# Kernel tuning notes

Hardware: AMD Instinct MI355X
Metric: run time of the kernel (lower is better)

The kernel has to match this reference:

```python
import jax, jax.numpy as jnp
import numpy as np

N = 100000   # nodes
E = 1600000  # edges (avg degree 16)
D = 128      # in_channels == hidden_channels
H = 4        # heads
C = D // H   # per-head channels = 32


def leaky(x, slope):
    return jnp.where(x >= 0, x, slope * x)


def setup_inputs() -> dict:
    key = jax.random.key(0)
    ks = jax.random.split(key, 12)
    s = 1.0 / np.sqrt(D)
    return {
        "x": jax.random.normal(ks[0], (N, D), jnp.float32),
        "edge_index": jax.random.randint(ks[1], (2, E), 0, N, jnp.int32),
        "edge_type": jax.random.randint(ks[2], (E,), 0, 8, jnp.int32),
        # linear1 (first_layer=True): LeakyReLU(0.01) -> Linear(D, D)
        "W1": jax.random.normal(ks[3], (D, D), jnp.float32) * s,
        "b1": jnp.zeros((D,), jnp.float32),
        # GATConv params: lin (no bias), att_src/att_dst [1,H,C], output bias [H*C]
        "Wg": jax.random.normal(ks[4], (D, D), jnp.float32) * s,
        "att_src": jax.random.normal(ks[5], (1, H, C), jnp.float32) * s,
        "att_dst": jax.random.normal(ks[6], (1, H, C), jnp.float32) * s,
        "bias_g": jnp.zeros((D,), jnp.float32),
        # linear2: LeakyReLU(0.01) -> Linear(D, D)
        "W2": jax.random.normal(ks[7], (D, D), jnp.float32) * s,
        "b2": jnp.zeros((D,), jnp.float32),
    }


def reference(x, edge_index, edge_type, W1, b1, Wg, att_src, att_dst, bias_g, W2, b2):
    # dropout layers act in eval mode (identity); edge_type is unused by forward.
    # linear1: LeakyReLU(0.01) then Linear
    x = leaky(x, 0.01) @ W1.T + b1                      # [N, D]

    # GATConv (add_self_loops=False, concat heads)
    h = (x @ Wg.T).reshape(N, H, C)                     # [N, H, C]
    a_src = jnp.sum(h * att_src, axis=-1)               # [N, H]
    a_dst = jnp.sum(h * att_dst, axis=-1)               # [N, H]

    src, dst = edge_index[0], edge_index[1]
    alpha = leaky(a_src[src] + a_dst[dst], 0.2)          # [E, H]

    # segment softmax over destination nodes (numerically stable)
    amax = jax.ops.segment_max(alpha, dst, num_segments=N)   # [N, H], -inf for empty
    amax = jnp.where(jnp.isfinite(amax), amax, 0.0)
    ex = jnp.exp(alpha - amax[dst])                      # [E, H]
    denom = jax.ops.segment_sum(ex, dst, num_segments=N) # [N, H]
    coeff = ex / (denom[dst] + 1e-16)                    # [E, H]

    msg = h[src] * coeff[:, :, None]                     # [E, H, C]
    out = jax.ops.segment_sum(msg, dst, num_segments=N)  # [N, H, C]
    out = out.reshape(N, H * C) + bias_g                 # [N, D]

    # linear2: LeakyReLU(0.01) then Linear; Dropout(0.3) identity at eval
    out = leaky(out, 0.01) @ W2.T + b2                   # [N, D]
    return out
```

## Files before the change

kernel.cpp:

```cpp
#include <hip/hip_runtime.h>
#include <hip/hip_bf16.h>

#define D128 128

typedef __attribute__((ext_vector_type(8))) short bf16x8;
typedef __attribute__((ext_vector_type(4))) float f32x4;

__device__ __forceinline__ float b2f(unsigned short u) {
    union { unsigned int i; float f; } z;
    z.i = ((unsigned int)u) << 16;
    return z.f;
}

__device__ __forceinline__ unsigned short f2b(float f) {
    union { float f; unsigned int i; } z;
    z.f = f;
    unsigned int r = z.i + 0x7FFFu + ((z.i >> 16) & 1u);
    return (unsigned short)(r >> 16);
}

__device__ __forceinline__ f32x4 mfma16(bf16x8 a, bf16x8 b, f32x4 c) {
    return __builtin_amdgcn_mfma_f32_16x16x32_bf16(a, b, c, 0, 0, 0);
}

#define CHUNK 8192
#define MAXBINS 512
#define BINCAP 8192
#define XBB 1536

__global__ __launch_bounds__(256) void k_prep1(
    const float* __restrict__ x,
    const float* __restrict__ W1, const float* __restrict__ Wg,
    const float* __restrict__ b1,
    const int* __restrict__ ei, int* __restrict__ M,
    float* __restrict__ Wc, float* __restrict__ bc,
    unsigned short* __restrict__ xb,
    int N, int E, int B, int nbins)
{
    __shared__ float wgr[256];
    __shared__ int hist[MAXBINS];
    const int t = threadIdx.x;
    if (blockIdx.x < 64) {
        const int i0 = blockIdx.x * 2;
        wgr[t] = Wg[i0 * 128 + t];
        __syncthreads();
        const int half = t >> 7;
        const int j = t & 127;
        const float* wr = &wgr[half * 128];
        float acc = 0.f;
        #pragma unroll 4
        for (int k = 0; k < 128; ++k)
            acc += wr[k] * W1[k * 128 + j];
        Wc[(i0 + half) * 128 + j] = acc;
        if (j == 0) {
            float ab = 0.f;
            for (int k = 0; k < 128; ++k) ab += wr[k] * b1[k];
            bc[i0 + half] = ab;
        }
    } else if (blockIdx.x < 64 + B) {
        const int chunk = blockIdx.x - 64;
        for (int i = t; i < nbins; i += 256) hist[i] = 0;
        __syncthreads();
        const int base = chunk * CHUNK;
        const int end = min(base + CHUNK, E);
        for (int e = base + t; e < end; e += 256)
            atomicAdd(&hist[ei[E + e] >> 8], 1);
        __syncthreads();
        for (int i = t; i < nbins; i += 256)
            M[i * B + chunk] = hist[i];
    } else {
        const size_t total = (size_t)N * 128;
        const size_t stride = (size_t)XBB * 256 * 8;
        for (size_t i = ((size_t)(blockIdx.x - 64 - B) * 256 + t) * 8; i + 8 <= total; i += stride) {
            float4 f0 = *(const float4*)(x + i);
            float4 f1 = *(const float4*)(x + i + 4);
            float v[8] = { f0.x, f0.y, f0.z, f0.w, f1.x, f1.y, f1.z, f1.w };
            union { uint4 q; unsigned short s[8]; } o;
            #pragma unroll
            for (int jj = 0; jj < 8; ++jj) {
                float f = v[jj];
                f = f >= 0.f ? f : 0.01f * f;
                o.s[jj] = f2b(f);
            }
            *(uint4*)(xb + i) = o.q;
        }
    }
}

__global__ __launch_bounds__(256) void k_prep2(
    const float* __restrict__ Wc, const float* __restrict__ bc,
    const float* __restrict__ att_s, const float* __restrict__ att_d,
    const float* __restrict__ W2,
    unsigned short* __restrict__ Wcat, unsigned short* __restrict__ W2l,
    float* __restrict__ lbias)
{
    const int b = blockIdx.x, t = threadIdx.x;
    if (b < 9) {
        const int q = b * 256 + t;
        const int ct = q >> 8, rem = q & 255;
        const int ks = rem >> 6, lane = rem & 63;
        const int ldiv = lane >> 4, lmod = lane & 15;
        const int kb = ks * 32 + ldiv * 8;
        float v[8];
        if (ct < 8) {
            const int rho = ct * 16 + lmod;
            const float4 a = *(const float4*)(Wc + rho * 128 + kb);
            const float4 bq = *(const float4*)(Wc + rho * 128 + kb + 4);
            v[0] = a.x; v[1] = a.y; v[2] = a.z; v[3] = a.w;
            v[4] = bq.x; v[5] = bq.y; v[6] = bq.z; v[7] = bq.w;
        } else {
            #pragma unroll
            for (int e = 0; e < 8; ++e) v[e] = 0.f;
            if (lmod < 8) {
                const int hh = lmod & 3;
                const float* av = lmod < 4 ? att_s : att_d;
                for (int c = 0; c < 32; ++c) {
                    const float w = av[hh * 32 + c];
                    const float* wrow = Wc + (hh * 32 + c) * 128 + kb;
                    #pragma unroll
                    for (int e = 0; e < 8; ++e) v[e] += w * wrow[e];
                }
            }
        }
        union { uint4 qq; unsigned short s[8]; } o;
        #pragma unroll
        for (int e = 0; e < 8; ++e) o.s[e] = f2b(v[e]);
        *(uint4*)(Wcat + q * 8) = o.qq;
    } else if (b < 17) {
        const int q = (b - 9) * 256 + t;
        const int ct = q >> 8, rem = q & 255;
        const int ks = rem >> 6, lane = rem & 63;
        const int ldiv = lane >> 4, lmod = lane & 15;
        const int kb = ks * 32 + ldiv * 8;
        const int rho = ct * 16 + lmod;
        const float4 a = *(const float4*)(W2 + rho * 128 + kb);
        const float4 bq = *(const float4*)(W2 + rho * 128 + kb + 4);
        union { uint4 qq; unsigned short s[8]; } o;
        o.s[0] = f2b(a.x); o.s[1] = f2b(a.y); o.s[2] = f2b(a.z); o.s[3] = f2b(a.w);
        o.s[4] = f2b(bq.x); o.s[5] = f2b(bq.y); o.s[6] = f2b(bq.z); o.s[7] = f2b(bq.w);
        *(uint4*)(W2l + q * 8) = o.qq;
    } else {
        if (t < 144) {
            float v = 0.f;
            if (t < 128) v = bc[t];
            else if (t < 136) {
                const int hh = (t - 128) & 3;
                const float* av = t < 132 ? att_s : att_d;
                for (int c = 0; c < 32; ++c) v += av[hh * 32 + c] * bc[hh * 32 + c];
            }
            lbias[t] = v;
        }
    }
}

__global__ __launch_bounds__(256) void k_gemm_h(
    const unsigned short* __restrict__ xb,
    const unsigned short* __restrict__ Wcat,
    const float* __restrict__ lbias,
    unsigned short* __restrict__ hfeat,
    float* __restrict__ asrc, float* __restrict__ adst, int N)
{
    __shared__ __align__(16) unsigned short sW[18432];
    const int t = threadIdx.x;
    const int wave = t >> 6, lane = t & 63, lmod = lane & 15, ldiv = lane >> 4;
    const int rowBase = blockIdx.x * 64;

    uint4 w[9];
    #pragma unroll
    for (int r = 0; r < 9; ++r)
        w[r] = *(const uint4*)(Wcat + r * 2048 + t * 8);

    int row = rowBase + wave * 16 + lmod;
    row = min(row, N - 1);
    bf16x8 afr[4];
    #pragma unroll
    for (int ks = 0; ks < 4; ++ks)
        afr[ks] = *(const bf16x8*)(xb + (size_t)row * D128 + ks * 32 + ldiv * 8);

    #pragma unroll
    for (int r = 0; r < 9; ++r)
        *(uint4*)&sW[r * 2048 + t * 8] = w[r];
    __syncthreads();

    f32x4 acc[9] = {};
    #pragma unroll
    for (int ct = 0; ct < 9; ++ct) {
        #pragma unroll
        for (int ks = 0; ks < 4; ++ks) {
            bf16x8 bfr = *(const bf16x8*)&sW[(ct * 256 + ks * 64 + lane) * 8];
            acc[ct] = mfma16(afr[ks], bfr, acc[ct]);
        }
    }

    const int orow = rowBase + wave * 16 + ldiv * 4;
    #pragma unroll
    for (int ct = 0; ct < 8; ++ct) {
        const int col = ct * 16 + lmod;
        const float bias = lbias[col];
        #pragma unroll
        for (int r = 0; r < 4; ++r)
            if (orow + r < N)
                hfeat[(size_t)(orow + r) * D128 + col] = f2b(acc[ct][r] + bias);
    }
    if (lmod < 8) {
        const float lb = lbias[128 + lmod];
        float* dst = lmod < 4 ? asrc : adst;
        const int hh = lmod & 3;
        #pragma unroll
        for (int r = 0; r < 4; ++r)
            if (orow + r < N)
                dst[(size_t)(orow + r) * 4 + hh] = acc[8][r] + lb;
    }
}

__global__ __launch_bounds__(1024) void k_scan1(
    const int* __restrict__ in, int* __restrict__ scanned,
    int* __restrict__ bsum, int n)
{
    __shared__ int lds[1024];
    const int gid = blockIdx.x * 1024 + threadIdx.x;
    const int v = gid < n ? in[gid] : 0;
    lds[threadIdx.x] = v;
    __syncthreads();
    #pragma unroll
    for (int off = 1; off < 1024; off <<= 1) {
        int t = threadIdx.x >= off ? lds[threadIdx.x - off] : 0;
        __syncthreads();
        lds[threadIdx.x] += t;
        __syncthreads();
    }
    if (gid < n) scanned[gid] = lds[threadIdx.x] - v;
    if (threadIdx.x == 1023) bsum[blockIdx.x] = lds[1023];
}

__global__ __launch_bounds__(256) void kA2(
    const int* __restrict__ ei, const int* __restrict__ scanned,
    const int* __restrict__ bsum, int2* __restrict__ binned,
    int E, int B, int nbins, int nM)
{
    __shared__ int cursor[MAXBINS];
    __shared__ int bpre[1024];
    const int nsb = (nM + 1023) >> 10;
    for (int i = threadIdx.x; i < nsb; i += 256) bpre[i] = bsum[i];
    __syncthreads();
    if (threadIdx.x == 0) {
        int run = 0;
        for (int i = 0; i < nsb; ++i) { int tv = bpre[i]; bpre[i] = run; run += tv; }
    }
    __syncthreads();
    for (int i = threadIdx.x; i < nbins; i += 256) {
        const int idx = i * B + blockIdx.x;
        cursor[i] = scanned[idx] + bpre[idx >> 10];
    }
    __syncthreads();
    const int base = blockIdx.x * CHUNK;
    const int end = min(base + CHUNK, E);
    for (int e = base + threadIdx.x; e < end; e += 256) {
        const int s = ei[e], d = ei[E + e];
        const int pos = atomicAdd(&cursor[d >> 8], 1);
        binned[pos] = make_int2(s, d);
    }
}

__global__ __launch_bounds__(256) void kB(
    const int2* __restrict__ binned, const int* __restrict__ scanned,
    const int* __restrict__ bsum, int* __restrict__ bucket,
    int* __restrict__ rowstart, int* __restrict__ rowend,
    int E, int B, int nbins, int N, int nM)
{
    __shared__ int2 eb[BINCAP];
    __shared__ int ldeg[256];
    __shared__ int lscan[256];
    __shared__ int lcur[256];
    __shared__ int bpre[1024];
    const int nsb = (nM + 1023) >> 10;
    for (int i = threadIdx.x; i < nsb; i += 256) bpre[i] = bsum[i];
    __syncthreads();
    if (threadIdx.x == 0) {
        int run = 0;
        for (int i = 0; i < nsb; ++i) { int tv = bpre[i]; bpre[i] = run; run += tv; }
    }
    __syncthreads();
    const int bin = blockIdx.x;
    const int i0 = bin * B;
    const int binstart = scanned[i0] + bpre[i0 >> 10];
    int binend;
    if (bin + 1 < nbins) {
        const int i1 = (bin + 1) * B;
        binend = scanned[i1] + bpre[i1 >> 10];
    } else {
        binend = E;
    }
    int n = binend - binstart;
    if (n > BINCAP) n = BINCAP;

    for (int i = threadIdx.x; i < n; i += 256) eb[i] = binned[binstart + i];
    ldeg[threadIdx.x] = 0;
    __syncthreads();
    for (int i = threadIdx.x; i < n; i += 256)
        atomicAdd(&ldeg[eb[i].y & 255], 1);
    __syncthreads();
    const int v = ldeg[threadIdx.x];
    lscan[threadIdx.x] = v;
    __syncthreads();
    #pragma unroll
    for (int off = 1; off < 256; off <<= 1) {
        int t = threadIdx.x >= off ? lscan[threadIdx.x - off] : 0;
        __syncthreads();
        lscan[threadIdx.x] += t;
        __syncthreads();
    }
    const int excl = lscan[threadIdx.x] - v;
    lcur[threadIdx.x] = excl;
    const int d = (bin << 8) + threadIdx.x;
    if (d < N) {
        rowstart[d] = binstart + excl;
        rowend[d]   = binstart + excl + v;
    }
    __syncthreads();
    for (int i = threadIdx.x; i < n; i += 256) {
        const int lp = atomicAdd(&lcur[eb[i].y & 255], 1);
        bucket[binstart + lp] = eb[i].x;
    }
}

__global__ __launch_bounds__(256) void k_gat(
    const int* __restrict__ bucket,
    const int* __restrict__ rowstart, const int* __restrict__ rowend,
    const float* __restrict__ asrc, const float* __restrict__ adst,
    const unsigned short* __restrict__ hfeat,
    const float* __restrict__ bias_g,
    unsigned short* __restrict__ outbf, int N)
{
    const int wave = threadIdx.x >> 6;
    const int lane = threadIdx.x & 63;
    const int g    = lane >> 4;
    const int gl   = lane & 15;
    const int h    = gl >> 2;
    const int d    = blockIdx.x * 16 + wave * 4 + g;

    int start = 0, end = 0;
    float a_d = 0.f;
    if (d < N) {
        start = rowstart[d];
        end   = rowend[d];
        a_d   = adst[(size_t)d * 4 + h];
    }
    const unsigned int chb = (unsigned int)(gl << 3);
    const unsigned short* hbase = hfeat + chb;

    float acc[8] = {0.f, 0.f, 0.f, 0.f, 0.f, 0.f, 0.f, 0.f};
    float denom = 0.f;

    int j = start;
    for (; j + 4 <= end; j += 4) {
        const int s0 = bucket[j];
        const int s1 = bucket[j + 1];
        const int s2 = bucket[j + 2];
        const int s3 = bucket[j + 3];
        const float as0 = asrc[((size_t)s0 << 2) + h];
        const float as1 = asrc[((size_t)s1 << 2) + h];
        const float as2 = asrc[((size_t)s2 << 2) + h];
        const float as3 = asrc[((size_t)s3 << 2) + h];
        const uint4 hp0 = *(const uint4*)(hbase + ((unsigned int)s0 << 7));
        const uint4 hp1 = *(const uint4*)(hbase + ((unsigned int)s1 << 7));
        const uint4 hp2 = *(const uint4*)(hbase + ((unsigned int)s2 << 7));
        const uint4 hp3 = *(const uint4*)(hbase + ((unsigned int)s3 << 7));
        float a0 = as0 + a_d; a0 = a0 >= 0.f ? a0 : 0.2f * a0;
        float a1 = as1 + a_d; a1 = a1 >= 0.f ? a1 : 0.2f * a1;
        float a2 = as2 + a_d; a2 = a2 >= 0.f ? a2 : 0.2f * a2;
        float a3 = as3 + a_d; a3 = a3 >= 0.f ? a3 : 0.2f * a3;
        const float w0 = __expf(a0), w1 = __expf(a1);
        const float w2 = __expf(a2), w3 = __expf(a3);
        denom += (w0 + w1) + (w2 + w3);
        acc[0] += w0 * b2f((unsigned short)(hp0.x & 0xFFFFu)) + w1 * b2f((unsigned short)(hp1.x & 0xFFFFu))
                + w2 * b2f((unsigned short)(hp2.x & 0xFFFFu)) + w3 * b2f((unsigned short)(hp3.x & 0xFFFFu));
        acc[1] += w0 * b2f((unsigned short)(hp0.x >> 16))     + w1 * b2f((unsigned short)(hp1.x >> 16))
                + w2 * b2f((unsigned short)(hp2.x >> 16))     + w3 * b2f((unsigned short)(hp3.x >> 16));
        acc[2] += w0 * b2f((unsigned short)(hp0.y & 0xFFFFu)) + w1 * b2f((unsigned short)(hp1.y & 0xFFFFu))
                + w2 * b2f((unsigned short)(hp2.y & 0xFFFFu)) + w3 * b2f((unsigned short)(hp3.y & 0xFFFFu));
        acc[3] += w0 * b2f((unsigned short)(hp0.y >> 16))     + w1 * b2f((unsigned short)(hp1.y >> 16))
                + w2 * b2f((unsigned short)(hp2.y >> 16))     + w3 * b2f((unsigned short)(hp3.y >> 16));
        acc[4] += w0 * b2f((unsigned short)(hp0.z & 0xFFFFu)) + w1 * b2f((unsigned short)(hp1.z & 0xFFFFu))
                + w2 * b2f((unsigned short)(hp2.z & 0xFFFFu)) + w3 * b2f((unsigned short)(hp3.z & 0xFFFFu));
        acc[5] += w0 * b2f((unsigned short)(hp0.z >> 16))     + w1 * b2f((unsigned short)(hp1.z >> 16))
                + w2 * b2f((unsigned short)(hp2.z >> 16))     + w3 * b2f((unsigned short)(hp3.z >> 16));
        acc[6] += w0 * b2f((unsigned short)(hp0.w & 0xFFFFu)) + w1 * b2f((unsigned short)(hp1.w & 0xFFFFu))
                + w2 * b2f((unsigned short)(hp2.w & 0xFFFFu)) + w3 * b2f((unsigned short)(hp3.w & 0xFFFFu));
        acc[7] += w0 * b2f((unsigned short)(hp0.w >> 16))     + w1 * b2f((unsigned short)(hp1.w >> 16))
                + w2 * b2f((unsigned short)(hp2.w >> 16))     + w3 * b2f((unsigned short)(hp3.w >> 16));
    }
    for (; j < end; ++j) {
        const int s0 = bucket[j];
        const float as0 = asrc[((size_t)s0 << 2) + h];
        const uint4 hp0 = *(const uint4*)(hbase + ((unsigned int)s0 << 7));
        float a0 = as0 + a_d; a0 = a0 >= 0.f ? a0 : 0.2f * a0;
        const float w0 = __expf(a0);
        denom += w0;
        acc[0] += w0 * b2f((unsigned short)(hp0.x & 0xFFFFu));
        acc[1] += w0 * b2f((unsigned short)(hp0.x >> 16));
        acc[2] += w0 * b2f((unsigned short)(hp0.y & 0xFFFFu));
        acc[3] += w0 * b2f((unsigned short)(hp0.y >> 16));
        acc[4] += w0 * b2f((unsigned short)(hp0.z & 0xFFFFu));
        acc[5] += w0 * b2f((unsigned short)(hp0.z >> 16));
        acc[6] += w0 * b2f((unsigned short)(hp0.w & 0xFFFFu));
        acc[7] += w0 * b2f((unsigned short)(hp0.w >> 16));
    }

    if (d < N) {
        const float inv = 1.f / (denom + 1e-16f);
        const float4 bg0 = *(const float4*)(bias_g + chb);
        const float4 bg1 = *(const float4*)(bias_g + chb + 4);
        const float bg[8] = { bg0.x, bg0.y, bg0.z, bg0.w, bg1.x, bg1.y, bg1.z, bg1.w };
        unsigned short s[8];
        #pragma unroll
        for (int k2 = 0; k2 < 8; ++k2) {
            float v = acc[k2] * inv + bg[k2];
            v = v >= 0.f ? v : 0.01f * v;
            s[k2] = f2b(v);
        }
        uint4 o;
        o.x = ((unsigned int)s[1] << 16) | s[0];
        o.y = ((unsigned int)s[3] << 16) | s[2];
        o.z = ((unsigned int)s[5] << 16) | s[4];
        o.w = ((unsigned int)s[7] << 16) | s[6];
        *(uint4*)(outbf + (((unsigned int)d << 7) + chb)) = o;
    }
}

__global__ __launch_bounds__(256) void k_final(
    const unsigned short* __restrict__ gatbf,
    const unsigned short* __restrict__ W2l,
    const float* __restrict__ b2,
    float* __restrict__ out, int N)
{
    __shared__ __align__(16) unsigned short sW[16384];
    const int t = threadIdx.x;
    const int wave = t >> 6, lane = t & 63, lmod = lane & 15, ldiv = lane >> 4;
    const int rowBase = blockIdx.x * 64;

    uint4 w[8];
    #pragma unroll
    for (int r = 0; r < 8; ++r)
        w[r] = *(const uint4*)(W2l + r * 2048 + t * 8);

    int row = rowBase + wave * 16 + lmod;
    row = min(row, N - 1);
    bf16x8 afr[4];
    #pragma unroll
    for (int ks = 0; ks < 4; ++ks)
        afr[ks] = *(const bf16x8*)(gatbf + (size_t)row * D128 + ks * 32 + ldiv * 8);

    #pragma unroll
    for (int r = 0; r < 8; ++r)
        *(uint4*)&sW[r * 2048 + t * 8] = w[r];
    __syncthreads();

    f32x4 acc[8] = {};
    #pragma unroll
    for (int ct = 0; ct < 8; ++ct) {
        #pragma unroll
        for (int ks = 0; ks < 4; ++ks) {
            bf16x8 bfr = *(const bf16x8*)&sW[(ct * 256 + ks * 64 + lane) * 8];
            acc[ct] = mfma16(afr[ks], bfr, acc[ct]);
        }
    }

    const int orow = rowBase + wave * 16 + ldiv * 4;
    #pragma unroll
    for (int ct = 0; ct < 8; ++ct) {
        const int col = ct * 16 + lmod;
        const float bb = b2[col];
        #pragma unroll
        for (int r = 0; r < 4; ++r)
            if (orow + r < N)
                out[(size_t)(orow + r) * D128 + col] = acc[ct][r] + bb;
    }
}

extern "C" void kernel_launch(void* const* d_in, const int* in_sizes, int n_in,
                              void* d_out, int out_size, void* d_ws, size_t ws_size,
                              hipStream_t stream)
{
    const float* x    = (const float*)d_in[0];
    const int*   ei   = (const int*)d_in[1];
    const float* W1   = (const float*)d_in[3];
    const float* b1   = (const float*)d_in[4];
    const float* Wg   = (const float*)d_in[5];
    const float* atts = (const float*)d_in[6];
    const float* attd = (const float*)d_in[7];
    const float* bg   = (const float*)d_in[8];
    const float* W2   = (const float*)d_in[9];
    const float* b2   = (const float*)d_in[10];
    float* out = (float*)d_out;

    const int N = in_sizes[0] / D128;
    const int E = in_sizes[1] / 2;

    const int B     = (E + CHUNK - 1) / CHUNK;
    const int nbins = (N + 255) >> 8;
    const int nM    = nbins * B;

    char* ws = (char*)d_ws;
    float* Wc = (float*)ws;
    size_t off = 65536;
    float* bc    = (float*)(ws + off); off += 512;
    float* lbias = (float*)(ws + off); off += 1024;
    unsigned short* Wcat = (unsigned short*)(ws + off); off += 36864;
    unsigned short* W2l  = (unsigned short*)(ws + off); off += 32768;
    unsigned short* xb   = (unsigned short*)(ws + off); off += (size_t)N * D128 * 2;
    unsigned short* hfeat = (unsigned short*)(ws + off); off += (size_t)N * D128 * 2;
    float* asrc = (float*)(ws + off); off += (size_t)N * 4 * 4;
    float* adst = (float*)(ws + off); off += (size_t)N * 4 * 4;
    int* M       = (int*)(ws + off); off += (size_t)nM * 4;
    int* scanned = (int*)(ws + off); off += (size_t)nM * 4;
    int* bsum    = (int*)(ws + off); off += 1024 * 4;
    int2* binned = (int2*)(ws + off); off += (size_t)E * 8;
    int* bucket  = (int*)(ws + off); off += (size_t)E * 4;
    int* rowstart = (int*)(ws + off); off += (size_t)N * 4;
    int* rowend   = (int*)(ws + off); off += (size_t)N * 4;
    unsigned short* outbf = (unsigned short*)(ws + off); off += (size_t)N * D128 * 2;

    k_prep1<<<64 + B + XBB, 256, 0, stream>>>(x, W1, Wg, b1, ei, M, Wc, bc, xb,
                                              N, E, B, nbins);
    k_prep2<<<18, 256, 0, stream>>>(Wc, bc, atts, attd, W2, Wcat, W2l, lbias);

    const int nbg = (N + 63) / 64;
    k_gemm_h<<<nbg, 256, 0, stream>>>(xb, Wcat, lbias, hfeat, asrc, adst, N);

    const int nsb = (nM + 1023) / 1024;
    k_scan1<<<nsb, 1024, 0, stream>>>(M, scanned, bsum, nM);
    kA2<<<B, 256, 0, stream>>>(ei, scanned, bsum, binned, E, B, nbins, nM);
    kB<<<nbins, 256, 0, stream>>>(binned, scanned, bsum, bucket,
                                  rowstart, rowend, E, B, nbins, N, nM);

    k_gat<<<(N + 15) / 16, 256, 0, stream>>>(bucket, rowstart, rowend,
                                             asrc, adst, hfeat, bg, outbf, N);

    k_final<<<nbg, 256, 0, stream>>>(outbf, W2l, b2, out, N);
}
```

Baseline: 302.6 us.

## Merge scan into prep2, merge GEMM with edge binning, unroll-by-2 GAT loop

The scan kernel is folded into the weight-prep kernel as extra 256-thread blocks that each scan 1024 entries, four per thread. The h-projection GEMM and the edge-binning pass are fused into one launch that dispatches on block index. This removes two kernel launches and lets independent work overlap. The GAT aggregation loop goes from 4-way to 2-way unrolling with nontemporal bucket loads, trading memory-level parallelism for fewer registers, and the fused kernel's 36KB LDS footprint also applies to the binning blocks.

```diff
diff --git a/kernel.cpp b/kernel.cpp
--- a/kernel.cpp
+++ b/kernel.cpp
@@ -87,13 +87,16 @@
     }
 }
 
-__global__ __launch_bounds__(256) void k_prep2(
+__global__ __launch_bounds__(256) void k_prep2s(
     const float* __restrict__ Wc, const float* __restrict__ bc,
     const float* __restrict__ att_s, const float* __restrict__ att_d,
     const float* __restrict__ W2,
     unsigned short* __restrict__ Wcat, unsigned short* __restrict__ W2l,
-    float* __restrict__ lbias)
-{
+    float* __restrict__ lbias,
+    const int* __restrict__ M, int* __restrict__ scanned,
+    int* __restrict__ bsum, int nM)
+{
+    __shared__ int lds[256];
     const int b = blockIdx.x, t = threadIdx.x;
     if (b < 9) {
         const int q = b * 256 + t;
@@ -139,7 +142,7 @@
         o.s[0] = f2b(a.x); o.s[1] = f2b(a.y); o.s[2] = f2b(a.z); o.s[3] = f2b(a.w);
         o.s[4] = f2b(bq.x); o.s[5] = f2b(bq.y); o.s[6] = f2b(bq.z); o.s[7] = f2b(bq.w);
         *(uint4*)(W2l + q * 8) = o.qq;
-    } else {
+    } else if (b == 17) {
         if (t < 144) {
             float v = 0.f;
             if (t < 128) v = bc[t];
@@ -150,115 +153,122 @@
             }
             lbias[t] = v;
         }
-    }
-}
-
-__global__ __launch_bounds__(256) void k_gemm_h(
+    } else {
+        const int sid = b - 18;
+        const int g0 = sid * 1024 + t * 4;
+        int v0 = g0     < nM ? M[g0]     : 0;
+        int v1 = g0 + 1 < nM ? M[g0 + 1] : 0;
+        int v2 = g0 + 2 < nM ? M[g0 + 2] : 0;
+        int v3 = g0 + 3 < nM ? M[g0 + 3] : 0;
+        const int s = v0 + v1 + v2 + v3;
+        lds[t] = s;
+        __syncthreads();
+        #pragma unroll
+        for (int off = 1; off < 256; off <<= 1) {
+            int tv = t >= off ? lds[t - off] : 0;
+            __syncthreads();
+            lds[t] += tv;
+            __syncthreads();
+        }
+        int run = lds[t] - s;
+        if (g0     < nM) scanned[g0]     = run;
+        run += v0;
+        if (g0 + 1 < nM) scanned[g0 + 1] = run;
+        run += v1;
+        if (g0 + 2 < nM) scanned[g0 + 2] = run;
+        run += v2;
+        if (g0 + 3 < nM) scanned[g0 + 3] = run;
+        if (t == 255) bsum[sid] = lds[255];
+    }
+}
+
+__global__ __launch_bounds__(256) void k_gemmA2(
     const unsigned short* __restrict__ xb,
     const unsigned short* __restrict__ Wcat,
     const float* __restrict__ lbias,
     unsigned short* __restrict__ hfeat,
-    float* __restrict__ asrc, float* __restrict__ adst, int N)
-{
-    __shared__ __align__(16) unsigned short sW[18432];
-    const int t = threadIdx.x;
-    const int wave = t >> 6, lane = t & 63, lmod = lane & 15, ldiv = lane >> 4;
-    const int rowBase = blockIdx.x * 64;
-
-    uint4 w[9];
-    #pragma unroll
-    for (int r = 0; r < 9; ++r)
-        w[r] = *(const uint4*)(Wcat + r * 2048 + t * 8);
-
-    int row = rowBase + wave * 16 + lmod;
-    row = min(row, N - 1);
-    bf16x8 afr[4];
-    #pragma unroll
-    for (int ks = 0; ks < 4; ++ks)
-        afr[ks] = *(const bf16x8*)(xb + (size_t)row * D128 + ks * 32 + ldiv * 8);
-
-    #pragma unroll
-    for (int r = 0; r < 9; ++r)
-        *(uint4*)&sW[r * 2048 + t * 8] = w[r];
-    __syncthreads();
-
-    f32x4 acc[9] = {};
-    #pragma unroll
-    for (int ct = 0; ct < 9; ++ct) {
-        #pragma unroll
-        for (int ks = 0; ks < 4; ++ks) {
-            bf16x8 bfr = *(const bf16x8*)&sW[(ct * 256 + ks * 64 + lane) * 8];
-            acc[ct] = mfma16(afr[ks], bfr, acc[ct]);
-        }
-    }
-
-    const int orow = rowBase + wave * 16 + ldiv * 4;
-    #pragma unroll
-    for (int ct = 0; ct < 8; ++ct) {
-        const int col = ct * 16 + lmod;
-        const float bias = lbias[col];
-        #pragma unroll
-        for (int r = 0; r < 4; ++r)
-            if (orow + r < N)
-                hfeat[(size_t)(orow + r) * D128 + col] = f2b(acc[ct][r] + bias);
-    }
-    if (lmod < 8) {
-        const float lb = lbias[128 + lmod];
-        float* dst = lmod < 4 ? asrc : adst;
-        const int hh = lmod & 3;
-        #pragma unroll
-        for (int r = 0; r < 4; ++r)
-            if (orow + r < N)
-                dst[(size_t)(orow + r) * 4 + hh] = acc[8][r] + lb;
-    }
-}
-
-__global__ __launch_bounds__(1024) void k_scan1(
-    const int* __restrict__ in, int* __restrict__ scanned,
-    int* __restrict__ bsum, int n)
-{
-    __shared__ int lds[1024];
-    const int gid = blockIdx.x * 1024 + threadIdx.x;
-    const int v = gid < n ? in[gid] : 0;
-    lds[threadIdx.x] = v;
-    __syncthreads();
-    #pragma unroll
-    for (int off = 1; off < 1024; off <<= 1) {
-        int t = threadIdx.x >= off ? lds[threadIdx.x - off] : 0;
-        __syncthreads();
-        lds[threadIdx.x] += t;
-        __syncthreads();
-    }
-    if (gid < n) scanned[gid] = lds[threadIdx.x] - v;
-    if (threadIdx.x == 1023) bsum[blockIdx.x] = lds[1023];
-}
-
-__global__ __launch_bounds__(256) void kA2(
+    float* __restrict__ asrc, float* __restrict__ adst,
     const int* __restrict__ ei, const int* __restrict__ scanned,
     const int* __restrict__ bsum, int2* __restrict__ binned,
-    int E, int B, int nbins, int nM)
-{
-    __shared__ int cursor[MAXBINS];
-    __shared__ int bpre[1024];
-    const int nsb = (nM + 1023) >> 10;
-    for (int i = threadIdx.x; i < nsb; i += 256) bpre[i] = bsum[i];
-    __syncthreads();
-    if (threadIdx.x == 0) {
-        int run = 0;
-        for (int i = 0; i < nsb; ++i) { int tv = bpre[i]; bpre[i] = run; run += tv; }
-    }
-    __syncthreads();
-    for (int i = threadIdx.x; i < nbins; i += 256) {
-        const int idx = i * B + blockIdx.x;
-        cursor[i] = scanned[idx] + bpre[idx >> 10];
-    }
-    __syncthreads();
-    const int base = blockIdx.x * CHUNK;
-    const int end = min(base + CHUNK, E);
-    for (int e = base + threadIdx.x; e < end; e += 256) {
-        const int s = ei[e], d = ei[E + e];
-        const int pos = atomicAdd(&cursor[d >> 8], 1);
-        binned[pos] = make_int2(s, d);
+    int N, int E, int B, int nbins, int nM, int nbg)
+{
+    __shared__ __align__(16) unsigned char smem[36864];
+    const int t = threadIdx.x;
+    if (blockIdx.x < nbg) {
+        unsigned short* sW = (unsigned short*)smem;
+        const int wave = t >> 6, lane = t & 63, lmod = lane & 15, ldiv = lane >> 4;
+        const int rowBase = blockIdx.x * 64;
+
+        uint4 w[9];
+        #pragma unroll
+        for (int r = 0; r < 9; ++r)
+            w[r] = *(const uint4*)(Wcat + r * 2048 + t * 8);
+
+        int row = rowBase + wave * 16 + lmod;
+        row = min(row, N - 1);
+        bf16x8 afr[4];
+        #pragma unroll
+        for (int ks = 0; ks < 4; ++ks)
+            afr[ks] = *(const bf16x8*)(xb + (size_t)row * D128 + ks * 32 + ldiv * 8);
+
+        #pragma unroll
+        for (int r = 0; r < 9; ++r)
+            *(uint4*)&sW[r * 2048 + t * 8] = w[r];
+        __syncthreads();
+
+        f32x4 acc[9] = {};
+        #pragma unroll
+        for (int ct = 0; ct < 9; ++ct) {
+            #pragma unroll
+            for (int ks = 0; ks < 4; ++ks) {
+                bf16x8 bfr = *(const bf16x8*)&sW[(ct * 256 + ks * 64 + lane) * 8];
+                acc[ct] = mfma16(afr[ks], bfr, acc[ct]);
+            }
+        }
+
+        const int orow = rowBase + wave * 16 + ldiv * 4;
+        #pragma unroll
+        for (int ct = 0; ct < 8; ++ct) {
+            const int col = ct * 16 + lmod;
+            const float bias = lbias[col];
+            #pragma unroll
+            for (int r = 0; r < 4; ++r)
+                if (orow + r < N)
+                    hfeat[(size_t)(orow + r) * D128 + col] = f2b(acc[ct][r] + bias);
+        }
+        if (lmod < 8) {
+            const float lb = lbias[128 + lmod];
+            float* dst = lmod < 4 ? asrc : adst;
+            const int hh = lmod & 3;
+            #pragma unroll
+            for (int r = 0; r < 4; ++r)
+                if (orow + r < N)
+                    dst[(size_t)(orow + r) * 4 + hh] = acc[8][r] + lb;
+        }
+    } else {
+        int* cursor = (int*)smem;
+        int* bpre   = (int*)(smem + MAXBINS * 4);
+        const int chunk = blockIdx.x - nbg;
+        const int nsb = (nM + 1023) >> 10;
+        for (int i = t; i < nsb; i += 256) bpre[i] = bsum[i];
+        __syncthreads();
+        if (t == 0) {
+            int run = 0;
+            for (int i = 0; i < nsb; ++i) { int tv = bpre[i]; bpre[i] = run; run += tv; }
+        }
+        __syncthreads();
+        for (int i = t; i < nbins; i += 256) {
+            const int idx = i * B + chunk;
+            cursor[i] = scanned[idx] + bpre[idx >> 10];
+        }
+        __syncthreads();
+        const int base = chunk * CHUNK;
+        const int end = min(base + CHUNK, E);
+        for (int e = base + t; e < end; e += 256) {
+            const int s = ei[e], d = ei[E + e];
+            const int pos = atomicAdd(&cursor[d >> 8], 1);
+            binned[pos] = make_int2(s, d);
+        }
     }
 }
 
@@ -305,9 +315,9 @@
     __syncthreads();
     #pragma unroll
     for (int off = 1; off < 256; off <<= 1) {
-        int t = threadIdx.x >= off ? lscan[threadIdx.x - off] : 0;
-        __syncthreads();
-        lscan[threadIdx.x] += t;
+        int tv = threadIdx.x >= off ? lscan[threadIdx.x - off] : 0;
+        __syncthreads();
+        lscan[threadIdx.x] += tv;
         __syncthreads();
     }
     const int excl = lscan[threadIdx.x] - v;
@@ -353,45 +363,28 @@
     float denom = 0.f;
 
     int j = start;
-    for (; j + 4 <= end; j += 4) {
-        const int s0 = bucket[j];
-        const int s1 = bucket[j + 1];
-        const int s2 = bucket[j + 2];
-        const int s3 = bucket[j + 3];
+    for (; j + 2 <= end; j += 2) {
+        const int s0 = __builtin_nontemporal_load(bucket + j);
+        const int s1 = __builtin_nontemporal_load(bucket + j + 1);
         const float as0 = asrc[((size_t)s0 << 2) + h];
         const float as1 = asrc[((size_t)s1 << 2) + h];
-        const float as2 = asrc[((size_t)s2 << 2) + h];
-        const float as3 = asrc[((size_t)s3 << 2) + h];
         const uint4 hp0 = *(const uint4*)(hbase + ((unsigned int)s0 << 7));
         const uint4 hp1 = *(const uint4*)(hbase + ((unsigned int)s1 << 7));
-        const uint4 hp2 = *(const uint4*)(hbase + ((unsigned int)s2 << 7));
-        const uint4 hp3 = *(const uint4*)(hbase + ((unsigned int)s3 << 7));
         float a0 = as0 + a_d; a0 = a0 >= 0.f ? a0 : 0.2f * a0;
         float a1 = as1 + a_d; a1 = a1 >= 0.f ? a1 : 0.2f * a1;
-        float a2 = as2 + a_d; a2 = a2 >= 0.f ? a2 : 0.2f * a2;
-        float a3 = as3 + a_d; a3 = a3 >= 0.f ? a3 : 0.2f * a3;
         const float w0 = __expf(a0), w1 = __expf(a1);
-        const float w2 = __expf(a2), w3 = __expf(a3);
-        denom += (w0 + w1) + (w2 + w3);
-        acc[0] += w0 * b2f((unsigned short)(hp0.x & 0xFFFFu)) + w1 * b2f((unsigned short)(hp1.x & 0xFFFFu))
-                + w2 * b2f((unsigned short)(hp2.x & 0xFFFFu)) + w3 * b2f((unsigned short)(hp3.x & 0xFFFFu));
-        acc[1] += w0 * b2f((unsigned short)(hp0.x >> 16))     + w1 * b2f((unsigned short)(hp1.x >> 16))
-                + w2 * b2f((unsigned short)(hp2.x >> 16))     + w3 * b2f((unsigned short)(hp3.x >> 16));
-        acc[2] += w0 * b2f((unsigned short)(hp0.y & 0xFFFFu)) + w1 * b2f((unsigned short)(hp1.y & 0xFFFFu))
-                + w2 * b2f((unsigned short)(hp2.y & 0xFFFFu)) + w3 * b2f((unsigned short)(hp3.y & 0xFFFFu));
-        acc[3] += w0 * b2f((unsigned short)(hp0.y >> 16))     + w1 * b2f((unsigned short)(hp1.y >> 16))
-                + w2 * b2f((unsigned short)(hp2.y >> 16))     + w3 * b2f((unsigned short)(hp3.y >> 16));
-        acc[4] += w0 * b2f((unsigned short)(hp0.z & 0xFFFFu)) + w1 * b2f((unsigned short)(hp1.z & 0xFFFFu))
-                + w2 * b2f((unsigned short)(hp2.z & 0xFFFFu)) + w3 * b2f((unsigned short)(hp3.z & 0xFFFFu));
-        acc[5] += w0 * b2f((unsigned short)(hp0.z >> 16))     + w1 * b2f((unsigned short)(hp1.z >> 16))
-                + w2 * b2f((unsigned short)(hp2.z >> 16))     + w3 * b2f((unsigned short)(hp3.z >> 16));
-        acc[6] += w0 * b2f((unsigned short)(hp0.w & 0xFFFFu)) + w1 * b2f((unsigned short)(hp1.w & 0xFFFFu))
-                + w2 * b2f((unsigned short)(hp2.w & 0xFFFFu)) + w3 * b2f((unsigned short)(hp3.w & 0xFFFFu));
-        acc[7] += w0 * b2f((unsigned short)(hp0.w >> 16))     + w1 * b2f((unsigned short)(hp1.w >> 16))
-                + w2 * b2f((unsigned short)(hp2.w >> 16))     + w3 * b2f((unsigned short)(hp3.w >> 16));
-    }
-    for (; j < end; ++j) {
-        const int s0 = bucket[j];
+        denom += w0 + w1;
+        acc[0] += w0 * b2f((unsigned short)(hp0.x & 0xFFFFu)) + w1 * b2f((unsigned short)(hp1.x & 0xFFFFu));
+        acc[1] += w0 * b2f((unsigned short)(hp0.x >> 16))     + w1 * b2f((unsigned short)(hp1.x >> 16));
+        acc[2] += w0 * b2f((unsigned short)(hp0.y & 0xFFFFu)) + w1 * b2f((unsigned short)(hp1.y & 0xFFFFu));
+        acc[3] += w0 * b2f((unsigned short)(hp0.y >> 16))     + w1 * b2f((unsigned short)(hp1.y >> 16));
+        acc[4] += w0 * b2f((unsigned short)(hp0.z & 0xFFFFu)) + w1 * b2f((unsigned short)(hp1.z & 0xFFFFu));
+        acc[5] += w0 * b2f((unsigned short)(hp0.z >> 16))     + w1 * b2f((unsigned short)(hp1.z >> 16));
+        acc[6] += w0 * b2f((unsigned short)(hp0.w & 0xFFFFu)) + w1 * b2f((unsigned short)(hp1.w & 0xFFFFu));
+        acc[7] += w0 * b2f((unsigned short)(hp0.w >> 16))     + w1 * b2f((unsigned short)(hp1.w >> 16));
+    }
+    if (j < end) {
+        const int s0 = __builtin_nontemporal_load(bucket + j);
         const float as0 = asrc[((size_t)s0 << 2) + h];
         const uint4 hp0 = *(const uint4*)(hbase + ((unsigned int)s0 << 7));
         float a0 = as0 + a_d; a0 = a0 >= 0.f ? a0 : 0.2f * a0;
@@ -500,6 +493,7 @@
     const int B     = (E + CHUNK - 1) / CHUNK;
     const int nbins = (N + 255) >> 8;
     const int nM    = nbins * B;
+    const int nsb   = (nM + 1023) / 1024;
 
     char* ws = (char*)d_ws;
     float* Wc = (float*)ws;
@@ -523,19 +517,15 @@
 
     k_prep1<<<64 + B + XBB, 256, 0, stream>>>(x, W1, Wg, b1, ei, M, Wc, bc, xb,
                                               N, E, B, nbins);
-    k_prep2<<<18, 256, 0, stream>>>(Wc, bc, atts, attd, W2, Wcat, W2l, lbias);
-
+    k_prep2s<<<18 + nsb, 256, 0, stream>>>(Wc, bc, atts, attd, W2, Wcat, W2l,
+                                           lbias, M, scanned, bsum, nM);
     const int nbg = (N + 63) / 64;
-    k_gemm_h<<<nbg, 256, 0, stream>>>(xb, Wcat, lbias, hfeat, asrc, adst, N);
-
-    const int nsb = (nM + 1023) / 1024;
-    k_scan1<<<nsb, 1024, 0, stream>>>(M, scanned, bsum, nM);
-    kA2<<<B, 256, 0, stream>>>(ei, scanned, bsum, binned, E, B, nbins, nM);
+    k_gemmA2<<<nbg + B, 256, 0, stream>>>(xb, Wcat, lbias, hfeat, asrc, adst,
+                                          ei, scanned, bsum, binned,
+                                          N, E, B, nbins, nM, nbg);
     kB<<<nbins, 256, 0, stream>>>(binned, scanned, bsum, bucket,
                                   rowstart, rowend, E, B, nbins, N, nM);
-
     k_gat<<<(N + 15) / 16, 256, 0, stream>>>(bucket, rowstart, rowend,
                                              asrc, adst, hfeat, bg, outbf, N);
-
     k_final<<<nbg, 256, 0, stream>>>(outbf, W2l, b2, out, N);
 }
```

Result: slower. 320.4 us (+5.9%).
